# Performance work log

Hardware: AMD Instinct MI355X
Metric: run time of the kernel (lower is better)

## Reference

```python
import jax, jax.numpy as jnp
import numpy as np

B, T, C, H = 2, 2048, 2048, 16
HD = C // H  # 128 head dim
ROPE_BASE = 10000.0


def setup_inputs() -> dict:
    key = jax.random.key(0)
    k0, k1, k2 = jax.random.split(key, 3)
    x = jax.random.normal(k0, (B, T, C), dtype=jnp.float32)
    W_attn = jax.random.normal(k1, (C, 3 * C), dtype=jnp.float32) * 0.02
    b_attn = jnp.zeros((3 * C,), dtype=jnp.float32)
    W_proj = jax.random.normal(k2, (C, C), dtype=jnp.float32) * 0.02
    b_proj = jnp.zeros((C,), dtype=jnp.float32)
    # freqs_cis = exp(i * t * theta_j), represented as (cos, sin), shape [T, HD//2]
    inv_freq = 1.0 / (ROPE_BASE ** (jnp.arange(0, HD, 2, dtype=jnp.float32) / HD))
    freqs = jnp.outer(jnp.arange(T, dtype=jnp.float32), inv_freq)
    return {"x": x, "W_attn": W_attn, "b_attn": b_attn, "W_proj": W_proj,
            "b_proj": b_proj, "cos": jnp.cos(freqs), "sin": jnp.sin(freqs)}


def _apply_rope(v, cos, sin):
    # v: [B, T, H, HD]; pairs (v[..., 2i], v[..., 2i+1]) rotated by angle freqs[t, i]
    vr = v.reshape(v.shape[:-1] + (-1, 2))
    x0, x1 = vr[..., 0], vr[..., 1]
    c = cos[None, :, None, :]  # [1, T, 1, HD//2]
    s = sin[None, :, None, :]
    o0 = x0 * c - x1 * s
    o1 = x0 * s + x1 * c
    return jnp.stack([o0, o1], axis=-1).reshape(v.shape)


def reference(x, W_attn, b_attn, W_proj, b_proj, cos, sin):
    Bv, Tv, Cv = x.shape
    qkv = x @ W_attn + b_attn                      # [B, T, 3C]
    q, k, v = jnp.split(qkv, 3, axis=-1)
    q = q.reshape(Bv, Tv, H, HD)
    k = k.reshape(Bv, Tv, H, HD)
    v = v.reshape(Bv, Tv, H, HD)
    q = _apply_rope(q, cos, sin)
    k = _apply_rope(k, cos, sin)
    scale = 1.0 / jnp.sqrt(jnp.float32(HD))
    att = jnp.einsum('bqhd,bkhd->bhqk', q, k) * scale
    causal = jnp.tril(jnp.ones((Tv, Tv), dtype=bool))
    att = jnp.where(causal[None, None], att, jnp.finfo(att.dtype).min)
    att = jax.nn.softmax(att, axis=-1)
    y = jnp.einsum('bhqk,bkhd->bqhd', att, v).reshape(Bv, Tv, Cv)
    return y @ W_proj + b_proj
```

## Files before the change

### kernel.cpp

```cpp
#include <hip/hip_runtime.h>

typedef unsigned short u16;
typedef __attribute__((ext_vector_type(8))) short short8;
typedef __attribute__((ext_vector_type(4))) float f32x4;

#define TSEQ 2048
#define NHEAD 16
#define HDIM 128

__device__ __forceinline__ u16 f2bf(float x) {
    unsigned u = __float_as_uint(x);
    return (u16)((u + 0x7fffu + ((u >> 16) & 1u)) >> 16);
}
__device__ __forceinline__ float b2f(u16 h) {
    return __uint_as_float(((unsigned)h) << 16);
}
__device__ __forceinline__ void async16(const void* g, void* l) {
    __builtin_amdgcn_global_load_lds((__attribute__((address_space(1))) void*)(void*)g,
                                     (__attribute__((address_space(3))) void*)l, 16, 0, 0);
}
__device__ __forceinline__ f32x4 zero4() {
    f32x4 z = {0.f, 0.f, 0.f, 0.f};
    return z;
}

template <int CTRL>
__device__ __forceinline__ float dppf(float x) {
    return __int_as_float(__builtin_amdgcn_mov_dpp(__float_as_int(x), CTRL, 0xf, 0xf, true));
}
__device__ __forceinline__ float dpp_max16(float x) {
    x = fmaxf(x, dppf<0xB1>(x));
    x = fmaxf(x, dppf<0x4E>(x));
    x = fmaxf(x, dppf<0x141>(x));
    x = fmaxf(x, dppf<0x140>(x));
    return x;
}
__device__ __forceinline__ float dpp_sum16(float x) {
    x += dppf<0xB1>(x);
    x += dppf<0x4E>(x);
    x += dppf<0x141>(x);
    x += dppf<0x140>(x);
    return x;
}

__global__ void cast_bf16(const float4* __restrict__ in, ushort4* __restrict__ out, int n4) {
    int i = blockIdx.x * 256 + threadIdx.x;
    if (i < n4) {
        float4 v = in[i];
        ushort4 o;
        o.x = f2bf(v.x); o.y = f2bf(v.y); o.z = f2bf(v.z); o.w = f2bf(v.w);
        out[i] = o;
    }
}

__global__ void transpose_cast(const float* __restrict__ in, u16* __restrict__ out, int K, int N) {
    __shared__ float tile[64][65];
    int n0 = blockIdx.x * 64, k0 = blockIdx.y * 64;
    int tx = threadIdx.x & 63, ty = threadIdx.x >> 6;
#pragma unroll
    for (int i = 0; i < 16; i++) {
        int r = ty + i * 4;
        tile[r][tx] = in[(size_t)(k0 + r) * N + n0 + tx];
    }
    __syncthreads();
#pragma unroll
    for (int i = 0; i < 16; i++) {
        int r = ty + i * 4;
        out[(size_t)(n0 + r) * K + k0 + tx] = f2bf(tile[tx][r]);
    }
}

#define WAIT_DS()                                          \
    {                                                      \
        asm volatile("s_waitcnt lgkmcnt(0)" ::: "memory"); \
        __builtin_amdgcn_sched_barrier(0);                 \
    }
#define BAR() __builtin_amdgcn_s_barrier();
#define VBAR_(N)                                               \
    {                                                          \
        asm volatile("s_waitcnt vmcnt(" #N ")" ::: "memory");  \
        __builtin_amdgcn_s_barrier();                          \
    }
#define VBAR(N) VBAR_(N)

#define STAGE(GP, GROW0, LB, KT)                                                                 \
    {                                                                                            \
        const u16* g0__ = (GP) + (size_t)((GROW0) + wave * 16 + grow) * (size_t)K + (KT)*64 +    \
                          gslot * 8;                                                             \
        u16* l0__ = (LB) + wave * 1024;                                                          \
        async16(g0__, l0__);                                                                     \
        async16(g0__ + (size_t)8 * K, l0__ + 512);                                               \
    }

#define LDA4(BASE, MB)                                                              \
    {                                                                               \
        _Pragma("unroll") for (int mm = 0; mm < 4; ++mm) {                          \
            a[mm][0] = *(const short8*)((BASE) + aoff0 + ((MB) + mm) * 1024);       \
            a[mm][1] = *(const short8*)((BASE) + aoff1 + ((MB) + mm) * 1024);       \
        }                                                                           \
    }
#define LDB2(BASE, NB)                                                              \
    {                                                                               \
        _Pragma("unroll") for (int nn = 0; nn < 2; ++nn) {                          \
            b[(NB) + nn][0] = *(const short8*)((BASE) + boff0 + ((NB) + nn) * 1024);\
            b[(NB) + nn][1] = *(const short8*)((BASE) + boff1 + ((NB) + nn) * 1024);\
        }                                                                           \
    }
#define MFQ(MB, NB)                                                                                   \
    {                                                                                                 \
        _Pragma("unroll") for (int mm = 0; mm < 4; ++mm) _Pragma("unroll") for (int nn = 0; nn < 2;   \
                                                                                ++nn) {               \
            acc[(MB) + mm][(NB) + nn] = __builtin_amdgcn_mfma_f32_16x16x32_bf16(                      \
                a[mm][0], b[(NB) + nn][0], acc[(MB) + mm][(NB) + nn], 0, 0, 0);                       \
            acc[(MB) + mm][(NB) + nn] = __builtin_amdgcn_mfma_f32_16x16x32_bf16(                      \
                a[mm][1], b[(NB) + nn][1], acc[(MB) + mm][(NB) + nn], 0, 0, 0);                       \
        }                                                                                             \
    }
#define PRIO_MFQ(MB, NB)                \
    {                                   \
        __builtin_amdgcn_s_setprio(1);  \
        MFQ(MB, NB);                    \
        __builtin_amdgcn_s_setprio(0);  \
    }

__global__ __launch_bounds__(512, 2) void gemm256(
    const u16* __restrict__ A, const u16* __restrict__ Bt, const float* __restrict__ bias,
    u16* __restrict__ qb, u16* __restrict__ kb, u16* __restrict__ vT,
    const float* __restrict__ cosp, const float* __restrict__ sinp,
    int M, int N, int K) {
    extern __shared__ u16 sm[];
    u16* const smA0 = sm;
    u16* const smB0 = sm + 16384;
    u16* const smA1 = sm + 32768;
    u16* const smB1 = sm + 49152;

    const int tid = threadIdx.x;
    const int wave = tid >> 6, lane = tid & 63;
    const int low = lane & 15, quad = lane >> 4;
    const int wr = wave >> 2, wc = wave & 3;
    const int m0 = blockIdx.y * 256, n0 = blockIdx.x * 256;
    const int NT = K >> 6;

    const int grow = lane >> 3;
    const int gslot = (lane & 7) ^ grow;

    const int swz = low & 7;
    const int arow = (wr * 128 + low) * 64;
    const int brow = (wc * 64 + low) * 64;
    const int aoff0 = arow + ((0 + quad) ^ swz) * 8;
    const int aoff1 = arow + ((4 + quad) ^ swz) * 8;
    const int boff0 = brow + ((0 + quad) ^ swz) * 8;
    const int boff1 = brow + ((4 + quad) ^ swz) * 8;

    f32x4 acc[8][4];
#pragma unroll
    for (int i = 0; i < 8; i++)
#pragma unroll
        for (int j = 0; j < 4; j++) acc[i][j] = zero4();
    short8 a[4][2], b[4][2];

    STAGE(A, m0, smA0, 0);
    STAGE(A, m0 + 128, smA0 + 8192, 0);
    STAGE(Bt, n0, smB0, 0);
    STAGE(Bt, n0 + 128, smB0 + 8192, 0);
    STAGE(A, m0, smA1, 1);
    STAGE(A, m0 + 128, smA1 + 8192, 1);
    STAGE(Bt, n0, smB1, 1);
    STAGE(Bt, n0 + 128, smB1 + 8192, 1);
    VBAR(8);

    const int NI = (NT >> 1) - 1;
#pragma unroll 1
    for (int it = 0; it < NI; ++it) {
        const int e = it * 2;
        LDA4(smA0, 0);
        LDB2(smB0, 0);
        LDB2(smB0, 2);
        PRIO_MFQ(0, 0);
        PRIO_MFQ(0, 2);
        LDA4(smA0, 4);
        WAIT_DS();
        BAR();
        PRIO_MFQ(4, 2);
        STAGE(A, m0, smA0, e + 2);
        STAGE(Bt, n0, smB0, e + 2);
        PRIO_MFQ(4, 0);
        VBAR(4);
        LDA4(smA1, 0);
        LDB2(smB1, 0);
        LDB2(smB1, 2);
        STAGE(A, m0 + 128, smA0 + 8192, e + 2);
        STAGE(Bt, n0 + 128, smB0 + 8192, e + 2);
        PRIO_MFQ(0, 0);
        PRIO_MFQ(0, 2);
        LDA4(smA1, 4);
        WAIT_DS();
        BAR();
        PRIO_MFQ(4, 2);
        STAGE(A, m0, smA1, e + 3);
        STAGE(A, m0 + 128, smA1 + 8192, e + 3);
        STAGE(Bt, n0, smB1, e + 3);
        STAGE(Bt, n0 + 128, smB1 + 8192, e + 3);
        PRIO_MFQ(4, 0);
        VBAR(8);
    }
    LDA4(smA0, 0);
    LDB2(smB0, 0);
    LDB2(smB0, 2);
    PRIO_MFQ(0, 0);
    PRIO_MFQ(0, 2);
    LDA4(smA0, 4);
    PRIO_MFQ(4, 2);
    PRIO_MFQ(4, 0);
    VBAR(0);
    LDA4(smA1, 0);
    LDB2(smB1, 0);
    LDB2(smB1, 2);
    PRIO_MFQ(0, 0);
    PRIO_MFQ(0, 2);
    LDA4(smA1, 4);
    PRIO_MFQ(4, 2);
    PRIO_MFQ(4, 0);

    __syncthreads();

    const int which = n0 >> 11;
    const int h0 = (n0 & 2047) >> 7;
    const int bb = m0 >> 11, t0 = m0 & 2047;
    float bvv[4];
#pragma unroll
    for (int nn = 0; nn < 4; ++nn) bvv[nn] = bias[n0 + wc * 64 + nn * 16 + low];

    if (which < 2) {
        u16* dstb = (which == 0 ? qb : kb);
        u16* epi = sm;
#pragma unroll
        for (int hh = 0; hh < 2; ++hh) {
            if ((wc >> 1) == hh) {
#pragma unroll
                for (int mm = 0; mm < 8; ++mm)
#pragma unroll
                    for (int nn = 0; nn < 4; ++nn)
#pragma unroll
                        for (int rr = 0; rr < 4; ++rr)
                            epi[(wr * 128 + mm * 16 + quad * 4 + rr) * 136 +
                                (wc & 1) * 64 + nn * 16 + low] = f2bf(acc[mm][nn][rr] + bvv[nn]);
            }
            __syncthreads();
            {
                const int row = tid >> 1, dh = (tid & 1) * 64;
                const int t = t0 + row;
                u16* dr = dstb + (((size_t)(bb * NHEAD + h0 + hh)) * TSEQ + t) * HDIM + dh;
                u16 vals[64];
#pragma unroll
                for (int qq = 0; qq < 8; ++qq)
                    *(short8*)(vals + qq * 8) = *(const short8*)(epi + row * 136 + dh + qq * 8);
                float csv[32], snv[32];
#pragma unroll
                for (int qq = 0; qq < 8; ++qq) {
                    *(float4*)(csv + qq * 4) =
                        *(const float4*)(cosp + (size_t)t * 64 + (dh >> 1) + qq * 4);
                    *(float4*)(snv + qq * 4) =
                        *(const float4*)(sinp + (size_t)t * 64 + (dh >> 1) + qq * 4);
                }
                u16 ov[64];
#pragma unroll
                for (int pp = 0; pp < 32; ++pp) {
                    float x0 = b2f(vals[2 * pp]), x1 = b2f(vals[2 * pp + 1]);
                    ov[2 * pp] = f2bf(x0 * csv[pp] - x1 * snv[pp]);
                    ov[2 * pp + 1] = f2bf(x0 * snv[pp] + x1 * csv[pp]);
                }
#pragma unroll
                for (int qq = 0; qq < 8; ++qq)
                    *(short8*)(dr + qq * 8) = *(const short8*)(ov + qq * 8);
            }
            __syncthreads();
        }
    } else {
        u16* epi = sm;
#pragma unroll
        for (int hh = 0; hh < 2; ++hh) {
            if ((wc >> 1) == hh) {
#pragma unroll
                for (int mm = 0; mm < 8; ++mm)
#pragma unroll
                    for (int nn = 0; nn < 4; ++nn)
#pragma unroll
                        for (int rr = 0; rr < 4; ++rr)
                            epi[((wc & 1) * 64 + nn * 16 + low) * 264 +
                                wr * 128 + mm * 16 + quad * 4 + rr] = f2bf(acc[mm][nn][rr] + bvv[nn]);
            }
            __syncthreads();
            {
                const int dd = tid >> 2, tc = (tid & 3) * 64;
                u16* dr = vT + ((size_t)(bb * NHEAD + h0 + hh) * HDIM + dd) * TSEQ + t0 + tc;
#pragma unroll
                for (int qq = 0; qq < 8; ++qq)
                    *(short8*)(dr + qq * 8) = *(const short8*)(epi + dd * 264 + tc + qq * 8);
            }
            __syncthreads();
        }
    }
}

#define PMFQ(NB)                                                                                      \
    {                                                                                                 \
        _Pragma("unroll") for (int mm = 0; mm < 4; ++mm) _Pragma("unroll") for (int nn = 0; nn < 2;   \
                                                                                ++nn) {               \
            acc[mm][(NB) + nn] = __builtin_amdgcn_mfma_f32_16x16x32_bf16(                             \
                a[mm][0], b[(NB) + nn][0], acc[mm][(NB) + nn], 0, 0, 0);                              \
            acc[mm][(NB) + nn] = __builtin_amdgcn_mfma_f32_16x16x32_bf16(                             \
                a[mm][1], b[(NB) + nn][1], acc[mm][(NB) + nn], 0, 0, 0);                              \
        }                                                                                             \
    }
#define PPRIO_MFQ(NB)                   \
    {                                   \
        __builtin_amdgcn_s_setprio(1);  \
        PMFQ(NB);                       \
        __builtin_amdgcn_s_setprio(0);  \
    }

__global__ __launch_bounds__(512, 2) void pgemm(
    const u16* __restrict__ A, const u16* __restrict__ Bt, const float* __restrict__ bias,
    float* __restrict__ outf, int M, int N, int K) {
    extern __shared__ u16 sm[];
    u16* const smA0 = sm;
    u16* const smB0 = sm + 8192;
    u16* const smA1 = sm + 24576;
    u16* const smB1 = sm + 32768;

    const int tid = threadIdx.x;
    const int wave = tid >> 6, lane = tid & 63;
    const int low = lane & 15, quad = lane >> 4;
    const int wr = wave >> 2, wc = wave & 3;
    const int m0 = blockIdx.y * 128, n0 = blockIdx.x * 256;
    const int NT = K >> 6;

    const int grow = lane >> 3;
    const int gslot = (lane & 7) ^ grow;

    const int swz = low & 7;
    const int arow = (wr * 64 + low) * 64;
    const int brow = (wc * 64 + low) * 64;
    const int aoff0 = arow + ((0 + quad) ^ swz) * 8;
    const int aoff1 = arow + ((4 + quad) ^ swz) * 8;
    const int boff0 = brow + ((0 + quad) ^ swz) * 8;
    const int boff1 = brow + ((4 + quad) ^ swz) * 8;

    f32x4 acc[4][4];
#pragma unroll
    for (int i = 0; i < 4; i++)
#pragma unroll
        for (int j = 0; j < 4; j++) acc[i][j] = zero4();
    short8 a[4][2], b[4][2];

    STAGE(A, m0, smA0, 0);
    STAGE(Bt, n0, smB0, 0);
    STAGE(Bt, n0 + 128, smB0 + 8192, 0);
    STAGE(A, m0, smA1, 1);
    STAGE(Bt, n0, smB1, 1);
    STAGE(Bt, n0 + 128, smB1 + 8192, 1);
    VBAR(6);

    const int NI = (NT >> 1) - 1;
#pragma unroll 1
    for (int it = 0; it < NI; ++it) {
        const int e = it * 2;
        LDA4(smA0, 0);
        LDB2(smB0, 0);
        LDB2(smB0, 2);
        PPRIO_MFQ(0);
        WAIT_DS();
        BAR();
        STAGE(A, m0, smA0, e + 2);
        STAGE(Bt, n0, smB0, e + 2);
        STAGE(Bt, n0 + 128, smB0 + 8192, e + 2);
        PPRIO_MFQ(2);
        VBAR(6);
        LDA4(smA1, 0);
        LDB2(smB1, 0);
        LDB2(smB1, 2);
        PPRIO_MFQ(0);
        WAIT_DS();
        BAR();
        STAGE(A, m0, smA1, e + 3);
        STAGE(Bt, n0, smB1, e + 3);
        STAGE(Bt, n0 + 128, smB1 + 8192, e + 3);
        PPRIO_MFQ(2);
        VBAR(6);
    }
    LDA4(smA0, 0);
    LDB2(smB0, 0);
    LDB2(smB0, 2);
    PPRIO_MFQ(0);
    PPRIO_MFQ(2);
    VBAR(0);
    LDA4(smA1, 0);
    LDB2(smB1, 0);
    LDB2(smB1, 2);
    PPRIO_MFQ(0);
    PPRIO_MFQ(2);

    float bvv[4];
#pragma unroll
    for (int nn = 0; nn < 4; ++nn) bvv[nn] = bias[n0 + wc * 64 + nn * 16 + low];
#pragma unroll
    for (int mm = 0; mm < 4; ++mm) {
        const int rbase = m0 + wr * 64 + mm * 16 + quad * 4;
#pragma unroll
        for (int nn = 0; nn < 4; ++nn) {
            const int col = n0 + wc * 64 + nn * 16 + low;
#pragma unroll
            for (int r = 0; r < 4; ++r)
                outf[(size_t)(rbase + r) * N + col] = acc[mm][nn][r] + bvv[nn];
        }
    }
}

#define STAGE_KV(KT, SEL)                                                                   \
    {                                                                                       \
        const int kv0s = (KT) * 64;                                                         \
        _Pragma("unroll") for (int j = 0; j < 4; j++) {                                     \
            const int row = j * 16 + krow;                                                  \
            const int gc = kchunk ^ (row & 7);                                              \
            async16(Kb + (size_t)(kv0s + row) * HDIM + gc * 8,                              \
                    Ksb + (SEL)*8192 + row * 128 + kchunk * 8);                             \
        }                                                                                   \
        _Pragma("unroll") for (int j = 0; j < 4; j++) {                                     \
            const int d = j * 32 + vrow;                                                    \
            const int gc = vchunk ^ (d & 7);                                                \
            async16(Vb + (size_t)d * TSEQ + kv0s + gc * 8,                                  \
                    Vsb + (SEL)*8192 + d * 64 + vchunk * 8);                                \
        }                                                                                   \
    }

__global__ __launch_bounds__(256) void flash_attn(const u16* __restrict__ qb, const u16* __restrict__ kb,
                                                  const u16* __restrict__ vT, u16* __restrict__ y) {
    extern __shared__ u16 fsm[];
    u16* const Ksb = fsm;
    u16* const Vsb = fsm + 16384;
    u16* const Psb = fsm + 32768;
    const int tid = threadIdx.x;
    const int wave = tid >> 6, lane = tid & 63;
    const int low = lane & 15, quad = lane >> 4;
    const int bh = blockIdx.x;
    const int qt = 31 - blockIdx.y;
    const int q0 = qt * 64 + wave * 16;
    const float scale2 = 0.08838834764831845f * 1.44269504088896f;

    const u16* Qp = qb + ((size_t)bh * TSEQ + q0) * HDIM;
    short8 qf[4];
#pragma unroll
    for (int c = 0; c < 4; c++) qf[c] = *(const short8*)(Qp + (size_t)low * HDIM + c * 32 + quad * 8);

    f32x4 o[8];
#pragma unroll
    for (int d = 0; d < 8; d++) o[d] = zero4();
    float m_i[4], l_i[4];
#pragma unroll
    for (int r = 0; r < 4; r++) { m_i[r] = -1e30f; l_i[r] = 0.f; }

    const u16* Kb = kb + (size_t)bh * TSEQ * HDIM;
    const u16* Vb = vT + (size_t)bh * HDIM * TSEQ;
    u16* Pw = Psb + wave * 1152;
    const int ntiles = qt + 1;

    const int krow = tid >> 4, kchunk = tid & 15;
    const int vrow = tid >> 3, vchunk = tid & 7;

    STAGE_KV(0, 0);
    for (int kt = 0; kt < ntiles; ++kt) {
        const int kv0 = kt * 64;
        VBAR(0);
        if (kt + 1 < ntiles) STAGE_KV(kt + 1, (kt + 1) & 1);
        const u16* Kc = Ksb + (kt & 1) * 8192;
        const u16* Vc = Vsb + (kt & 1) * 8192;

        f32x4 s[4];
#pragma unroll
        for (int h = 0; h < 4; h++) s[h] = zero4();
        __builtin_amdgcn_s_setprio(1);
#pragma unroll
        for (int h = 0; h < 4; h++) {
            const int row = h * 16 + low;
#pragma unroll
            for (int c = 0; c < 4; c++) {
                const int cc = c * 4 + quad;
                short8 kf = *(const short8*)(Kc + row * 128 + (cc ^ (row & 7)) * 8);
                s[h] = __builtin_amdgcn_mfma_f32_16x16x32_bf16(qf[c], kf, s[h], 0, 0, 0);
            }
        }
        __builtin_amdgcn_s_setprio(0);

        float alpha[4];
#pragma unroll
        for (int r = 0; r < 4; r++) {
            const int qg = q0 + quad * 4 + r;
            float sv[4];
#pragma unroll
            for (int h = 0; h < 4; h++) sv[h] = s[h][r] * scale2;
            if (kt == qt) {
#pragma unroll
                for (int h = 0; h < 4; h++)
                    if (kv0 + h * 16 + low > qg) sv[h] = -1e30f;
            }
            float mx = fmaxf(fmaxf(sv[0], sv[1]), fmaxf(sv[2], sv[3]));
            mx = dpp_max16(mx);
            float mnew = fmaxf(m_i[r], mx);
            alpha[r] = exp2f(m_i[r] - mnew);
            m_i[r] = mnew;
            float p0 = exp2f(sv[0] - mnew);
            float p1 = exp2f(sv[1] - mnew);
            float p2 = exp2f(sv[2] - mnew);
            float p3 = exp2f(sv[3] - mnew);
            float rs = (p0 + p1) + (p2 + p3);
            rs = dpp_sum16(rs);
            l_i[r] = l_i[r] * alpha[r] + rs;
            const int prow = (quad * 4 + r) * 72;
            Pw[prow + low] = f2bf(p0);
            Pw[prow + 16 + low] = f2bf(p1);
            Pw[prow + 32 + low] = f2bf(p2);
            Pw[prow + 48 + low] = f2bf(p3);
        }
        __threadfence_block();

#pragma unroll
        for (int d = 0; d < 8; ++d)
#pragma unroll
            for (int r = 0; r < 4; r++) o[d][r] *= alpha[r];

        __builtin_amdgcn_s_setprio(1);
#pragma unroll
        for (int kc = 0; kc < 2; kc++) {
            short8 pf = *(const short8*)(Pw + low * 72 + kc * 32 + quad * 8);
#pragma unroll
            for (int dd = 0; dd < 8; ++dd) {
                const int vr = dd * 16 + low;
                const int cc = kc * 4 + quad;
                short8 vf = *(const short8*)(Vc + vr * 64 + (cc ^ (vr & 7)) * 8);
                o[dd] = __builtin_amdgcn_mfma_f32_16x16x32_bf16(pf, vf, o[dd], 0, 0, 0);
            }
        }
        __builtin_amdgcn_s_setprio(0);
    }

    const int b = bh >> 4, h = bh & 15;
#pragma unroll
    for (int r = 0; r < 4; r++) {
        float inv = 1.0f / l_i[r];
        size_t row = (size_t)(b * TSEQ + q0 + quad * 4 + r);
        u16* yp = y + row * 2048 + h * HDIM;
#pragma unroll
        for (int d = 0; d < 8; ++d) yp[d * 16 + low] = f2bf(o[d][r] * inv);
    }
}

extern "C" void kernel_launch(void* const* d_in, const int* in_sizes, int n_in,
                              void* d_out, int out_size, void* d_ws, size_t ws_size,
                              hipStream_t stream) {
    const float* x = (const float*)d_in[0];
    const float* Wa = (const float*)d_in[1];
    const float* ba = (const float*)d_in[2];
    const float* Wp = (const float*)d_in[3];
    const float* bp = (const float*)d_in[4];
    const float* cs = (const float*)d_in[5];
    const float* sn = (const float*)d_in[6];
    float* out = (float*)d_out;

    u16* xb = (u16*)d_ws;
    u16* Wab = xb + 8388608;
    u16* Wpb = Wab + 12582912;
    u16* qb = Wpb + 4194304;
    u16* kb = qb + 8388608;
    u16* vT = kb + 8388608;
    u16* y = xb;

    static bool attr_set = false;
    if (!attr_set) {
        hipFuncSetAttribute(reinterpret_cast<const void*>(gemm256),
                            hipFuncAttributeMaxDynamicSharedMemorySize, 131072);
        hipFuncSetAttribute(reinterpret_cast<const void*>(pgemm),
                            hipFuncAttributeMaxDynamicSharedMemorySize, 98304);
        hipFuncSetAttribute(reinterpret_cast<const void*>(flash_attn),
                            hipFuncAttributeMaxDynamicSharedMemorySize, 74752);
        attr_set = true;
    }

    cast_bf16<<<8192, 256, 0, stream>>>((const float4*)x, (ushort4*)xb, 2097152);
    transpose_cast<<<dim3(96, 32), 256, 0, stream>>>(Wa, Wab, 2048, 6144);
    transpose_cast<<<dim3(32, 32), 256, 0, stream>>>(Wp, Wpb, 2048, 2048);
    gemm256<<<dim3(24, 16), 512, 131072, stream>>>(xb, Wab, ba, qb, kb, vT, cs, sn, 4096, 6144, 2048);
    flash_attn<<<dim3(32, 32), 256, 74752, stream>>>(qb, kb, vT, y);
    pgemm<<<dim3(8, 32), 512, 98304, stream>>>(y, Wpb, bp, out, 4096, 2048, 2048);
}
```

Baseline: 399.5 us.

## Enlarge flash-attention query tile to 128 rows with 8 waves; fuse prep kernels

The flash attention kernel now uses 512 threads (8 waves), so each block covers 128 query rows and shares every staged K/V tile across twice as many waves. Global-to-LDS traffic per query row is roughly halved. Waves whose rows sit entirely above a KV tile skip that tile, and the causal mask is applied only on diagonal tiles. The three input cast/transpose kernels are merged into one launch, which removes launch overhead. The cost is idle waves on diagonal tiles, fewer blocks in the grid, and more LDS per block, which may reduce occupancy.

```diff
diff --git a/kernel.cpp b/kernel.cpp
--- a/kernel.cpp
+++ b/kernel.cpp
@@ -43,20 +43,34 @@
     return x;
 }
 
-__global__ void cast_bf16(const float4* __restrict__ in, ushort4* __restrict__ out, int n4) {
-    int i = blockIdx.x * 256 + threadIdx.x;
-    if (i < n4) {
-        float4 v = in[i];
+__global__ __launch_bounds__(256) void prep(
+    const float* __restrict__ x, u16* __restrict__ xb,
+    const float* __restrict__ Wa, u16* __restrict__ Wab,
+    const float* __restrict__ Wp, u16* __restrict__ Wpb) {
+    __shared__ float tile[64][65];
+    const int bx = blockIdx.x;
+    const int tid = threadIdx.x;
+    if (bx < 8192) {
+        int i = bx * 256 + tid;
+        float4 v = ((const float4*)x)[i];
         ushort4 o;
         o.x = f2bf(v.x); o.y = f2bf(v.y); o.z = f2bf(v.z); o.w = f2bf(v.w);
-        out[i] = o;
-    }
-}
-
-__global__ void transpose_cast(const float* __restrict__ in, u16* __restrict__ out, int K, int N) {
-    __shared__ float tile[64][65];
-    int n0 = blockIdx.x * 64, k0 = blockIdx.y * 64;
-    int tx = threadIdx.x & 63, ty = threadIdx.x >> 6;
+        ((ushort4*)xb)[i] = o;
+        return;
+    }
+    const float* in;
+    u16* out;
+    int K, N, n0, k0;
+    if (bx < 11264) {
+        const int bid = bx - 8192;
+        in = Wa; out = Wab; K = 2048; N = 6144;
+        n0 = (bid % 96) * 64; k0 = (bid / 96) * 64;
+    } else {
+        const int bid = bx - 11264;
+        in = Wp; out = Wpb; K = 2048; N = 2048;
+        n0 = (bid % 32) * 64; k0 = (bid / 32) * 64;
+    }
+    const int tx = tid & 63, ty = tid >> 6;
 #pragma unroll
     for (int i = 0; i < 16; i++) {
         int r = ty + i * 4;
@@ -420,22 +434,24 @@
 #define STAGE_KV(KT, SEL)                                                                   \
     {                                                                                       \
         const int kv0s = (KT) * 64;                                                         \
-        _Pragma("unroll") for (int j = 0; j < 4; j++) {                                     \
-            const int row = j * 16 + krow;                                                  \
-            const int gc = kchunk ^ (row & 7);                                              \
-            async16(Kb + (size_t)(kv0s + row) * HDIM + gc * 8,                              \
-                    Ksb + (SEL)*8192 + row * 128 + kchunk * 8);                             \
+        _Pragma("unroll") for (int q = 0; q < 2; q++) {                                     \
+            const int blk = q * 8 + wave;                                                   \
+            const int kr = blk * 4 + (lane >> 4);                                           \
+            const int kgc = (lane & 15) ^ (kr & 7);                                         \
+            async16(Kb + (size_t)(kv0s + kr) * HDIM + kgc * 8,                              \
+                    Ksb + (SEL)*8192 + blk * 512 + lane * 8);                               \
         }                                                                                   \
-        _Pragma("unroll") for (int j = 0; j < 4; j++) {                                     \
-            const int d = j * 32 + vrow;                                                    \
-            const int gc = vchunk ^ (d & 7);                                                \
-            async16(Vb + (size_t)d * TSEQ + kv0s + gc * 8,                                  \
-                    Vsb + (SEL)*8192 + d * 64 + vchunk * 8);                                \
+        _Pragma("unroll") for (int q = 0; q < 2; q++) {                                     \
+            const int blk = q * 8 + wave;                                                   \
+            const int dv = blk * 8 + (lane >> 3);                                           \
+            const int vgc = (lane & 7) ^ (dv & 7);                                          \
+            async16(Vb + (size_t)dv * TSEQ + kv0s + vgc * 8,                                \
+                    Vsb + (SEL)*8192 + blk * 512 + lane * 8);                               \
         }                                                                                   \
     }
 
-__global__ __launch_bounds__(256) void flash_attn(const u16* __restrict__ qb, const u16* __restrict__ kb,
-                                                  const u16* __restrict__ vT, u16* __restrict__ y) {
+__global__ __launch_bounds__(512, 2) void flash_attn(const u16* __restrict__ qb, const u16* __restrict__ kb,
+                                                     const u16* __restrict__ vT, u16* __restrict__ y) {
     extern __shared__ u16 fsm[];
     u16* const Ksb = fsm;
     u16* const Vsb = fsm + 16384;
@@ -444,8 +460,8 @@
     const int wave = tid >> 6, lane = tid & 63;
     const int low = lane & 15, quad = lane >> 4;
     const int bh = blockIdx.x;
-    const int qt = 31 - blockIdx.y;
-    const int q0 = qt * 64 + wave * 16;
+    const int qt = 15 - blockIdx.y;
+    const int q0 = qt * 128 + wave * 16;
     const float scale2 = 0.08838834764831845f * 1.44269504088896f;
 
     const u16* Qp = qb + ((size_t)bh * TSEQ + q0) * HDIM;
@@ -463,10 +479,7 @@
     const u16* Kb = kb + (size_t)bh * TSEQ * HDIM;
     const u16* Vb = vT + (size_t)bh * HDIM * TSEQ;
     u16* Pw = Psb + wave * 1152;
-    const int ntiles = qt + 1;
-
-    const int krow = tid >> 4, kchunk = tid & 15;
-    const int vrow = tid >> 3, vchunk = tid & 7;
+    const int ntiles = 2 * qt + 2;
 
     STAGE_KV(0, 0);
     for (int kt = 0; kt < ntiles; ++kt) {
@@ -476,72 +489,75 @@
         const u16* Kc = Ksb + (kt & 1) * 8192;
         const u16* Vc = Vsb + (kt & 1) * 8192;
 
-        f32x4 s[4];
-#pragma unroll
-        for (int h = 0; h < 4; h++) s[h] = zero4();
-        __builtin_amdgcn_s_setprio(1);
-#pragma unroll
-        for (int h = 0; h < 4; h++) {
-            const int row = h * 16 + low;
-#pragma unroll
-            for (int c = 0; c < 4; c++) {
-                const int cc = c * 4 + quad;
-                short8 kf = *(const short8*)(Kc + row * 128 + (cc ^ (row & 7)) * 8);
-                s[h] = __builtin_amdgcn_mfma_f32_16x16x32_bf16(qf[c], kf, s[h], 0, 0, 0);
+        if (kv0 <= q0 + 15) {
+            f32x4 s[4];
+#pragma unroll
+            for (int h = 0; h < 4; h++) s[h] = zero4();
+            __builtin_amdgcn_s_setprio(1);
+#pragma unroll
+            for (int h = 0; h < 4; h++) {
+                const int row = h * 16 + low;
+#pragma unroll
+                for (int c = 0; c < 4; c++) {
+                    const int cc = c * 4 + quad;
+                    short8 kf = *(const short8*)(Kc + row * 128 + (cc ^ (row & 7)) * 8);
+                    s[h] = __builtin_amdgcn_mfma_f32_16x16x32_bf16(qf[c], kf, s[h], 0, 0, 0);
+                }
             }
+            __builtin_amdgcn_s_setprio(0);
+
+            const bool domask = (kv0 + 63 > q0);
+            float alpha[4];
+#pragma unroll
+            for (int r = 0; r < 4; r++) {
+                const int qg = q0 + quad * 4 + r;
+                float sv[4];
+#pragma unroll
+                for (int h = 0; h < 4; h++) sv[h] = s[h][r] * scale2;
+                if (domask) {
+#pragma unroll
+                    for (int h = 0; h < 4; h++)
+                        if (kv0 + h * 16 + low > qg) sv[h] = -1e30f;
+                }
+                float mx = fmaxf(fmaxf(sv[0], sv[1]), fmaxf(sv[2], sv[3]));
+                mx = dpp_max16(mx);
+                float mnew = fmaxf(m_i[r], mx);
+                alpha[r] = exp2f(m_i[r] - mnew);
+                m_i[r] = mnew;
+                float p0 = exp2f(sv[0] - mnew);
+                float p1 = exp2f(sv[1] - mnew);
+                float p2 = exp2f(sv[2] - mnew);
+                float p3 = exp2f(sv[3] - mnew);
+                float rs = (p0 + p1) + (p2 + p3);
+                rs = dpp_sum16(rs);
+                l_i[r] = l_i[r] * alpha[r] + rs;
+                const int prow = (quad * 4 + r) * 72;
+                Pw[prow + low] = f2bf(p0);
+                Pw[prow + 16 + low] = f2bf(p1);
+                Pw[prow + 32 + low] = f2bf(p2);
+                Pw[prow + 48 + low] = f2bf(p3);
+            }
+            __threadfence_block();
+
+#pragma unroll
+            for (int d = 0; d < 8; ++d)
+#pragma unroll
+                for (int r = 0; r < 4; r++) o[d][r] *= alpha[r];
+
+            __builtin_amdgcn_s_setprio(1);
+#pragma unroll
+            for (int kc = 0; kc < 2; kc++) {
+                short8 pf = *(const short8*)(Pw + low * 72 + kc * 32 + quad * 8);
+#pragma unroll
+                for (int dd = 0; dd < 8; ++dd) {
+                    const int vr = dd * 16 + low;
+                    const int cc = kc * 4 + quad;
+                    short8 vf = *(const short8*)(Vc + vr * 64 + (cc ^ (vr & 7)) * 8);
+                    o[dd] = __builtin_amdgcn_mfma_f32_16x16x32_bf16(pf, vf, o[dd], 0, 0, 0);
+                }
+            }
+            __builtin_amdgcn_s_setprio(0);
         }
-        __builtin_amdgcn_s_setprio(0);
-
-        float alpha[4];
-#pragma unroll
-        for (int r = 0; r < 4; r++) {
-            const int qg = q0 + quad * 4 + r;
-            float sv[4];
-#pragma unroll
-            for (int h = 0; h < 4; h++) sv[h] = s[h][r] * scale2;
-            if (kt == qt) {
-#pragma unroll
-                for (int h = 0; h < 4; h++)
-                    if (kv0 + h * 16 + low > qg) sv[h] = -1e30f;
-            }
-            float mx = fmaxf(fmaxf(sv[0], sv[1]), fmaxf(sv[2], sv[3]));
-            mx = dpp_max16(mx);
-            float mnew = fmaxf(m_i[r], mx);
-            alpha[r] = exp2f(m_i[r] - mnew);
-            m_i[r] = mnew;
-            float p0 = exp2f(sv[0] - mnew);
-            float p1 = exp2f(sv[1] - mnew);
-            float p2 = exp2f(sv[2] - mnew);
-            float p3 = exp2f(sv[3] - mnew);
-            float rs = (p0 + p1) + (p2 + p3);
-            rs = dpp_sum16(rs);
-            l_i[r] = l_i[r] * alpha[r] + rs;
-            const int prow = (quad * 4 + r) * 72;
-            Pw[prow + low] = f2bf(p0);
-            Pw[prow + 16 + low] = f2bf(p1);
-            Pw[prow + 32 + low] = f2bf(p2);
-            Pw[prow + 48 + low] = f2bf(p3);
-        }
-        __threadfence_block();
-
-#pragma unroll
-        for (int d = 0; d < 8; ++d)
-#pragma unroll
-            for (int r = 0; r < 4; r++) o[d][r] *= alpha[r];
-
-        __builtin_amdgcn_s_setprio(1);
-#pragma unroll
-        for (int kc = 0; kc < 2; kc++) {
-            short8 pf = *(const short8*)(Pw + low * 72 + kc * 32 + quad * 8);
-#pragma unroll
-            for (int dd = 0; dd < 8; ++dd) {
-                const int vr = dd * 16 + low;
-                const int cc = kc * 4 + quad;
-                short8 vf = *(const short8*)(Vc + vr * 64 + (cc ^ (vr & 7)) * 8);
-                o[dd] = __builtin_amdgcn_mfma_f32_16x16x32_bf16(pf, vf, o[dd], 0, 0, 0);
-            }
-        }
-        __builtin_amdgcn_s_setprio(0);
     }
 
     const int b = bh >> 4, h = bh & 15;
@@ -582,14 +598,12 @@
         hipFuncSetAttribute(reinterpret_cast<const void*>(pgemm),
                             hipFuncAttributeMaxDynamicSharedMemorySize, 98304);
         hipFuncSetAttribute(reinterpret_cast<const void*>(flash_attn),
-                            hipFuncAttributeMaxDynamicSharedMemorySize, 74752);
+                            hipFuncAttributeMaxDynamicSharedMemorySize, 83968);
         attr_set = true;
     }
 
-    cast_bf16<<<8192, 256, 0, stream>>>((const float4*)x, (ushort4*)xb, 2097152);
-    transpose_cast<<<dim3(96, 32), 256, 0, stream>>>(Wa, Wab, 2048, 6144);
-    transpose_cast<<<dim3(32, 32), 256, 0, stream>>>(Wp, Wpb, 2048, 2048);
+    prep<<<12288, 256, 0, stream>>>(x, xb, Wa, Wab, Wp, Wpb);
     gemm256<<<dim3(24, 16), 512, 131072, stream>>>(xb, Wab, ba, qb, kb, vT, cs, sn, 4096, 6144, 2048);
-    flash_attn<<<dim3(32, 32), 256, 74752, stream>>>(qb, kb, vT, y);
+    flash_attn<<<dim3(32, 16), 512, 83968, stream>>>(qb, kb, vT, y);
     pgemm<<<dim3(8, 32), 512, 98304, stream>>>(y, Wpb, bp, out, 4096, 2048, 2048);
 }
```

Measured after the change: 390.3 us. 2.3% less time.
